# Performance work log

Measured on AMD Instinct MI355X. Metric: run time of the kernel, lower is better.

The kernel has to match this reference:

```python
import jax, jax.numpy as jnp
import numpy as np

# --- static config (matches init_kwargs) ---
N = 30000            # n_nodes
H = 8                # num_heads
OT = 16              # out_time_dim
OS = 240             # out_space_dim
IN_DIM = 16 + 1 + 240   # in_time+1 + in_space = 257
OUT_DIM = OT + 1 + OS   # 257 per head
BETA = -1.0
EPS = 1e-8
MAX_NORM = 1.0e6
SQRT_BETA = float(np.sqrt(abs(BETA)))


def setup_inputs() -> dict:
    key = jax.random.key(0)
    ks = jax.random.split(key, 7)
    def w(k, shape, fan_in):
        return (jax.random.normal(k, shape, jnp.float32) / np.sqrt(fan_in)).astype(jnp.float32)
    return {
        "query_input": jax.random.normal(ks[0], (N, IN_DIM), jnp.float32),
        "source_input": jax.random.normal(ks[1], (N, IN_DIM), jnp.float32),
        # stacked per-head PseudoLinear2 weights: [H, out, in]
        "Wq": w(ks[2], (H, OUT_DIM, IN_DIM), IN_DIM),
        "Wk": w(ks[3], (H, OUT_DIM, IN_DIM), IN_DIM),
        "Wv": w(ks[4], (H, OUT_DIM, IN_DIM), IN_DIM),
        # final head-concat projections (nn.Linear, bias=False): [out, in]
        "Ws": w(ks[5], (OT + 1, H * (OT + 1)), H * (OT + 1)),
        "Wh": w(ks[6], (OS, H * OS), H * OS),
    }


def _pseudo_linear(x, W):
    # Per-head linear; spherical block renormalized to radius sqrt(|beta|)
    # (hr output on the product manifold S^OT x H^OS). [N,D] x [H,O,D] -> [N,H,O]
    y = jnp.einsum('nd,hod->nho', x, W)
    s, sp = y[..., :OT + 1], y[..., OT + 1:]
    s = s * (SQRT_BETA / (jnp.linalg.norm(s, axis=-1, keepdims=True) + EPS))
    return jnp.concatenate([s, sp], axis=-1)


def _linear_attention(q, k, v, den_eps):
    # elu+1 feature-map linear attention; associative kv outer product per head.
    phi_q = jax.nn.elu(q) + 1.0
    phi_k = jax.nn.elu(k) + 1.0
    ktv = jnp.einsum('nhm,nhd->hmd', phi_k, v)          # [H,m,d]
    num = jnp.einsum('nhm,hmd->nhd', phi_q, ktv)        # [N,H,d]
    den = jnp.einsum('nhd,hd->nh', phi_q, phi_k.sum(0)) # [N,H]
    return num / (den[..., None] + den_eps)


def _l2norm(x):
    # torch F.normalize(p=2, dim=-1)
    return x / jnp.clip(jnp.linalg.norm(x, axis=-1, keepdims=True), 1e-12)


def reference(query_input, source_input, Wq, Wk, Wv, Ws, Wh):
    q = _pseudo_linear(query_input, Wq)   # [N,H,257]
    k = _pseudo_linear(source_input, Wk)
    v = _pseudo_linear(source_input, Wv)
    qs, qh = q[..., :OT + 1], q[..., OT + 1:]
    ks_, kh = k[..., :OT + 1], k[..., OT + 1:]
    vs, vh = v[..., :OT + 1], v[..., OT + 1:]

    # ---- spherical linear attention ----
    a = _linear_attention(qs, ks_, vs, 1e-6)            # [N,H,OT+1]
    a = a.reshape(N, H * (OT + 1)) @ Ws.T               # heads_concat
    an = jnp.linalg.norm(a, axis=-1, keepdims=True) + EPS
    mask = (an > MAX_NORM).astype(a.dtype)
    an_c = jnp.minimum(an, MAX_NORM)
    a_ = (a / an_c) * mask + a * (1.0 - mask)
    att_s = SQRT_BETA * _l2norm(a_)                     # [N,OT+1]

    # ---- hyperbolic linear attention ----
    b = _linear_attention(qh, kh, vh, 1e-8)             # [N,H,OS]
    b = b.reshape(N, H * OS) @ Wh.T
    bn = jnp.linalg.norm(b, axis=-1, keepdims=True) + EPS
    maskb = (bn > MAX_NORM).astype(b.dtype)
    bn_c = jnp.minimum(bn, MAX_NORM)
    b_ = _l2norm(b / bn_c) * MAX_NORM
    b2 = b_ * maskb + b * (1.0 - maskb)
    bt = jnp.sqrt(bn_c ** 2 - BETA)                     # hyperbolic time coord
    att_h = jnp.concatenate([bt, b2], axis=-1)          # [N,OS+1]

    out = jnp.concatenate([att_s, att_h], axis=-1)      # [N,OT+1+OS+1]
    # sh_to_q: product S x H -> pseudo-hyperboloid Q; reverse_extrinsic_map = identity here.
    s_part, h_part = out[:, :OT + 1], out[:, OT + 1:]
    q_out = jnp.concatenate([h_part[:, :1] * s_part / SQRT_BETA, h_part[:, 1:]], axis=-1)
    return q_out  # [N, 257]
```

## Files before the change

kernel.cpp:

```cpp
#include <hip/hip_runtime.h>
#include <math.h>

typedef __bf16 bf16_t;
typedef __bf16 bf16x8 __attribute__((ext_vector_type(8)));
typedef float f32x4 __attribute__((ext_vector_type(4)));

#define H    8
#define SD   17
#define HD   240
#define KIN  257
#define KQP  288
#define SCOL 256
#define DTOT 2176
#define NTOT 30000
#define CHS  6000
#define NCS  5
#define CHPS 6144
#define CHQ  7500
#define CHQP 7552
#define NCQ  4
#define KSPLIT 16

#define BK   32

__device__ __forceinline__ float phi_elu1(float x) {
    return x > 0.f ? x + 1.f : __expf(x);
}

__device__ __forceinline__ int xcd_swz(int orig, int nwg) {
    int q = nwg >> 3, r = nwg & 7;
    int xcd = orig & 7, off = orig >> 3;
    return (xcd < r ? xcd * (q + 1) : r * (q + 1) + (xcd - r) * q) + off;
}

__device__ __forceinline__ void gl_lds16(const bf16_t* g, bf16_t* l) {
    __builtin_amdgcn_global_load_lds(
        (const __attribute__((address_space(1))) void*)g,
        (__attribute__((address_space(3))) void*)l, 16, 0, 0);
}

struct GemmP {
    const bf16_t* A; long lda; long aHead;
    const bf16_t* B; long ldb; long bHead;
    float* Cf; bf16_t* Cb; long ldc; long cHead; int atomicC;
    int M, N, K, nSplit;
};

template<int TBM, int TBN>
__global__ void __launch_bounds__(256)
k_mfma_nt(GemmP p)
{
    constexpr int FI = TBM / 32;
    constexpr int FJ = TBN / 32;
    __shared__ bf16_t As[2][TBM * BK];
    __shared__ bf16_t Bs[2][TBN * BK];
    const int t  = threadIdx.x;
    const int z  = blockIdx.z;
    const int h  = z / p.nSplit;
    const int sp = z % p.nSplit;
    const int kWin = p.K / p.nSplit;
    const int k0   = sp * kWin;
    const int nwg  = gridDim.x * gridDim.y;
    const int wg   = xcd_swz(blockIdx.y * gridDim.x + blockIdx.x, nwg);
    const int m0 = (wg % gridDim.x) * TBM;
    const int n0 = (wg / gridDim.x) * TBN;
    const bf16_t* A = p.A + (long)h * p.aHead;
    const bf16_t* B = p.B + (long)h * p.bHead;

    const int lr = t >> 2;
    const int lc = t & 3;
    const int wid  = t >> 6;
    const int lane = t & 63;
    const int wm = (wid >> 1) * (TBM / 2);
    const int wn = (wid & 1) * (TBN / 2);
    const int fr = lane & 15;
    const int fq = lane >> 4;

    f32x4 acc[FI][FJ] = {};

    auto stage = [&](int buf, int kb) {
        const int gk = kb + lc * 8;
#pragma unroll
        for (int it = 0; it < TBM / 64; ++it)
            gl_lds16(A + (long)(m0 + lr + it * 64) * p.lda + gk, &As[buf][it * 2048 + t * 8]);
#pragma unroll
        for (int it = 0; it < TBN / 64; ++it)
            gl_lds16(B + (long)(n0 + lr + it * 64) * p.ldb + gk, &Bs[buf][it * 2048 + t * 8]);
    };

    stage(0, k0);
    __syncthreads();
    int cur = 0;
    for (int kb = k0; kb < k0 + kWin; kb += BK) {
        if (kb + BK < k0 + kWin) stage(cur ^ 1, kb + BK);
        bf16x8 af[FI], bfr[FJ];
#pragma unroll
        for (int i = 0; i < FI; ++i)
            af[i] = *(const bf16x8*)(&As[cur][(wm + i * 16 + fr) * BK + fq * 8]);
#pragma unroll
        for (int j = 0; j < FJ; ++j)
            bfr[j] = *(const bf16x8*)(&Bs[cur][(wn + j * 16 + fr) * BK + fq * 8]);
#pragma unroll
        for (int i = 0; i < FI; ++i)
#pragma unroll
            for (int j = 0; j < FJ; ++j)
                acc[i][j] = __builtin_amdgcn_mfma_f32_16x16x32_bf16(af[i], bfr[j], acc[i][j], 0, 0, 0);
        __syncthreads();
        cur ^= 1;
    }

    float*  Cf = p.Cf ? p.Cf + (long)h * p.cHead : (float*)0;
    bf16_t* Cb = p.Cb ? p.Cb + (long)h * p.cHead : (bf16_t*)0;
#pragma unroll
    for (int i = 0; i < FI; ++i) {
#pragma unroll
        for (int r = 0; r < 4; ++r) {
            const int m = m0 + wm + i * 16 + fq * 4 + r;
            if (m >= p.M) continue;
#pragma unroll
            for (int j = 0; j < FJ; ++j) {
                const int n = n0 + wn + j * 16 + fr;
                if (n >= p.N) continue;
                const float v = acc[i][j][r];
                const long idx = (long)m * p.ldc + n;
                if (p.atomicC)      atomicAdd(&Cf[idx], v);
                else if (Cf)        Cf[idx] = v;
                else                Cb[idx] = (bf16_t)v;
            }
        }
    }
}

__global__ void __launch_bounds__(256)
k_mfma_kv(const bf16_t* __restrict__ A, const bf16_t* __restrict__ Bsrc,
          bf16_t* __restrict__ Tk, bf16_t* __restrict__ Tv,
          float* __restrict__ ksum, int nRows)
{
    constexpr int FI = 4, FJ = 4;
    __shared__ bf16_t As[2][128 * BK];
    __shared__ bf16_t Bs[2][128 * BK];
    const int t = threadIdx.x;
    const int nwg = gridDim.x * gridDim.y;
    const int wg  = xcd_swz(blockIdx.y * gridDim.x + blockIdx.x, nwg);
    const int m0 = (wg % gridDim.x) * 128;
    const int n0 = (wg / gridDim.x) * 128;

    const int lr = t >> 2;
    const int lc = t & 3;
    const int wid  = t >> 6;
    const int lane = t & 63;
    const int wm = (wid >> 1) * 64;
    const int wn = (wid & 1) * 64;
    const int fr = lane & 15;
    const int fq = lane >> 4;

    f32x4 acc[FI][FJ] = {};

    auto stage = [&](int buf, int kb) {
        const int gk = kb + lc * 8;
        gl_lds16(A    + (long)(m0 + lr)      * KQP + gk, &As[buf][t * 8]);
        gl_lds16(A    + (long)(m0 + lr + 64) * KQP + gk, &As[buf][2048 + t * 8]);
        gl_lds16(Bsrc + (long)(n0 + lr)      * KQP + gk, &Bs[buf][t * 8]);
        gl_lds16(Bsrc + (long)(n0 + lr + 64) * KQP + gk, &Bs[buf][2048 + t * 8]);
    };

    stage(0, 0);
    __syncthreads();
    int cur = 0;
    for (int kb = 0; kb < KQP; kb += BK) {
        if (kb + BK < KQP) stage(cur ^ 1, kb + BK);
        bf16x8 af[FI], bfr[FJ];
#pragma unroll
        for (int i = 0; i < FI; ++i)
            af[i] = *(const bf16x8*)(&As[cur][(wm + i * 16 + fr) * BK + fq * 8]);
#pragma unroll
        for (int j = 0; j < FJ; ++j)
            bfr[j] = *(const bf16x8*)(&Bs[cur][(wn + j * 16 + fr) * BK + fq * 8]);
#pragma unroll
        for (int i = 0; i < FI; ++i)
#pragma unroll
            for (int j = 0; j < FJ; ++j)
                acc[i][j] = __builtin_amdgcn_mfma_f32_16x16x32_bf16(af[i], bfr[j], acc[i][j], 0, 0, 0);
        __syncthreads();
        cur ^= 1;
    }

    const bool isKh = (m0 >= SCOL) && (m0 < DTOT);
    bf16_t* outB = (m0 < DTOT) ? (Tk + (long)m0 * CHPS)
                               : (Tv + (long)(m0 - DTOT) * CHPS);
#pragma unroll
    for (int i = 0; i < FI; ++i) {
#pragma unroll
        for (int r = 0; r < 4; ++r) {
            const int ml = wm + i * 16 + fq * 4 + r;
            bf16_t* row = outB + (long)ml * CHPS;
            float kacc = 0.f;
#pragma unroll
            for (int j = 0; j < FJ; ++j) {
                const int n = n0 + wn + j * 16 + fr;
                float v = 0.f;
                if (n < nRows) {
                    v = acc[i][j][r];
                    if (isKh) { v = phi_elu1(v); kacc += v; }
                }
                row[n] = (bf16_t)v;
            }
            if (isKh) {
                kacc += __shfl_xor(kacc, 1);
                kacc += __shfl_xor(kacc, 2);
                kacc += __shfl_xor(kacc, 4);
                kacc += __shfl_xor(kacc, 8);
                if (fr == 0) atomicAdd(&ksum[m0 + ml], kacc);
            }
        }
    }
}

__global__ void k_zero_tail(bf16_t* __restrict__ Tk, bf16_t* __restrict__ Tv)
{
    const int row = blockIdx.x;
    const int t = threadIdx.x;
    bf16_t* B = (t >= 128) ? Tv : Tk;
    B[(long)row * CHPS + (CHPS - 128) + (t & 127)] = (bf16_t)0.f;
}

__global__ void __launch_bounds__(256)
k_post_kv_t(bf16_t* __restrict__ Tk, bf16_t* __restrict__ Tv,
            float* __restrict__ ksum, int rows)
{
    const int h = blockIdx.y;
    const int n = blockIdx.x * 256 + threadIdx.x;
    const int lane = threadIdx.x & 63;
    const bool act = n < rows;
    float kv[SD], vv[SD];
    float sk = 0.f, sv = 0.f;
#pragma unroll
    for (int j = 0; j < SD; ++j) {
        kv[j] = act ? (float)Tk[(long)(h * 32 + j) * CHPS + n] : 0.f;
        vv[j] = act ? (float)Tv[(long)(h * 32 + j) * CHPS + n] : 0.f;
        sk += kv[j] * kv[j];
        sv += vv[j] * vv[j];
    }
    const float ik = 1.f / (sqrtf(sk) + 1e-8f);
    const float iv = 1.f / (sqrtf(sv) + 1e-8f);
#pragma unroll
    for (int j = 0; j < SD; ++j) {
        float pk = act ? phi_elu1(kv[j] * ik) : 0.f;
        if (act) {
            Tk[(long)(h * 32 + j) * CHPS + n] = (bf16_t)pk;
            Tv[(long)(h * 32 + j) * CHPS + n] = (bf16_t)(vv[j] * iv);
        }
        float s = pk;
#pragma unroll
        for (int off = 32; off > 0; off >>= 1) s += __shfl_down(s, off);
        if (lane == 0) atomicAdd(&ksum[h * 32 + j], s);
    }
}

__global__ void k_cast_pad(const float* __restrict__ in, bf16_t* __restrict__ out, long rows)
{
    long i = (long)blockIdx.x * 256 + threadIdx.x;
    if (i >= rows * KQP) return;
    long r = i / KQP; int k = (int)(i - r * KQP);
    out[i] = (k < KIN) ? (bf16_t)in[r * KIN + k] : (bf16_t)0.f;
}

__global__ void k_prep_proj(const float* __restrict__ W, bf16_t* __restrict__ dst)
{
    long i = (long)blockIdx.x * 256 + threadIdx.x;
    if (i >= (long)DTOT * KQP) return;
    int r = (int)(i / KQP), k = (int)(i % KQP);
    float v = 0.f;
    if (r < SCOL) {
        int h = r >> 5, j = r & 31;
        if (j < SD && k < KIN) v = W[((long)h * 257 + j) * 257 + k];
    } else {
        int rr = r - SCOL;
        int h = rr / HD, j = rr % HD;
        if (k < KIN) v = W[((long)h * 257 + SD + j) * 257 + k];
    }
    dst[i] = (bf16_t)v;
}

__global__ void k_prep_ws(const float* __restrict__ ws, bf16_t* __restrict__ out)
{
    int o = blockIdx.x; int t = threadIdx.x;
    int h = t >> 5, j = t & 31;
    float v = 0.f;
    if (o < SD && j < SD) v = ws[o * (H * SD) + h * SD + j];
    out[o * 256 + t] = (bf16_t)v;
}

__global__ void k_prep_wh(const float* __restrict__ wh, bf16_t* __restrict__ out)
{
    long i = (long)blockIdx.x * 256 + threadIdx.x;
    if (i >= 256L * 2048) return;
    int o = (int)(i / 2048), c = (int)(i % 2048);
    int h = c >> 8, j = c & 255;
    float v = 0.f;
    if (o < 240 && j < HD) v = wh[(long)o * 1920 + h * HD + j];
    out[i] = (bf16_t)v;
}

__global__ void __launch_bounds__(256)
k_post_q(bf16_t* __restrict__ Yq, const float* __restrict__ ksum, int rows)
{
    const int wid  = blockIdx.x * 4 + (threadIdx.x >> 6);
    const int lane = threadIdx.x & 63;
    const int n = wid >> 3, h = wid & 7;
    if (n >= rows) return;
    bf16_t* row = Yq + (long)n * DTOT;
    float qv = (lane < SD) ? (float)row[h * 32 + lane] : 0.f;
    float sq = qv * qv;
#pragma unroll
    for (int off = 32; off > 0; off >>= 1) sq += __shfl_down(sq, off);
    sq = __shfl(sq, 0);
    const float iq = 1.f / (sqrtf(sq) + 1e-8f);
    float pvs = (lane < SD) ? phi_elu1(qv * iq) : 0.f;
    float ds = (lane < SD) ? pvs * ksum[h * 32 + lane] : 0.f;
    float pvh[4];
    float dh = 0.f;
#pragma unroll
    for (int i = 0; i < 4; ++i) {
        int o = lane + 64 * i;
        if (o < HD) {
            pvh[i] = phi_elu1((float)row[SCOL + h * HD + o]);
            dh += pvh[i] * ksum[SCOL + h * HD + o];
        } else pvh[i] = 0.f;
    }
#pragma unroll
    for (int off = 32; off > 0; off >>= 1) {
        ds += __shfl_down(ds, off);
        dh += __shfl_down(dh, off);
    }
    ds = __shfl(ds, 0); dh = __shfl(dh, 0);
    const float ss = 1.f / (ds + 1e-6f);
    const float sh = 1.f / (dh + 1e-8f);
    if (lane < 32)
        row[h * 32 + lane] = (bf16_t)((lane < SD) ? pvs * ss : 0.f);
#pragma unroll
    for (int i = 0; i < 4; ++i) {
        int o = lane + 64 * i;
        if (o < HD) row[SCOL + h * HD + o] = (bf16_t)(pvh[i] * sh);
    }
}

__global__ void k_castf(const float* __restrict__ in, bf16_t* __restrict__ out, long n)
{
    long i = (long)blockIdx.x * 256 + threadIdx.x;
    if (i < n) out[i] = (bf16_t)in[i];
}

__global__ void __launch_bounds__(256)
k_finalize(const float* __restrict__ pre, float* __restrict__ outp, int rows)
{
    int n    = blockIdx.x * 4 + (threadIdx.x >> 6);
    int lane = threadIdx.x & 63;
    if (n >= rows) return;
    const float* rp = pre + (long)n * 257;
    float* op = outp + (long)n * 257;
    float sv = (lane < SD) ? rp[lane] : 0.f;
    float ssq = sv * sv;
    float hv[4];
    float hsq = 0.f;
#pragma unroll
    for (int i = 0; i < 4; ++i) {
        int o = lane + 64 * i;
        hv[i] = (o < HD) ? rp[SD + o] : 0.f;
        hsq += hv[i] * hv[i];
    }
#pragma unroll
    for (int off = 32; off > 0; off >>= 1) {
        ssq += __shfl_down(ssq, off);
        hsq += __shfl_down(hsq, off);
    }
    ssq = __shfl(ssq, 0); hsq = __shfl(hsq, 0);
    float an_raw = sqrtf(ssq);
    float bn_raw = sqrtf(hsq);
    float an = an_raw + 1e-8f;
    float bn = bn_raw + 1e-8f;
    bool ma = an > 1e6f;
    bool mb = bn > 1e6f;
    float an_c = fminf(an, 1e6f);
    float bn_c = fminf(bn, 1e6f);
    float na = ma ? (an_raw / an_c) : an_raw;
    na = fmaxf(na, 1e-12f);
    float inv_s = (ma ? (1.f / an_c) : 1.f) / na;
    float bt = sqrtf(bn_c * bn_c + 1.0f);
    float nb = fmaxf(bn_raw / bn_c, 1e-12f);
    float scale_b = 1e6f / (bn_c * nb);
    if (lane < SD) op[lane] = bt * (sv * inv_s);
#pragma unroll
    for (int i = 0; i < 4; ++i) {
        int o = lane + 64 * i;
        if (o < HD) op[SD + o] = mb ? hv[i] * scale_b : hv[i];
    }
}

static inline long alup(long b) { return (b + 255) & ~255L; }

extern "C" void kernel_launch(void* const* d_in, const int* in_sizes, int n_in,
                              void* d_out, int out_size, void* d_ws, size_t ws_size,
                              hipStream_t stream)
{
    const float* query  = (const float*)d_in[0];
    const float* source = (const float*)d_in[1];
    const float* Wq     = (const float*)d_in[2];
    const float* Wk     = (const float*)d_in[3];
    const float* Wv     = (const float*)d_in[4];
    const float* Ws     = (const float*)d_in[5];
    const float* Wh     = (const float*)d_in[6];
    float* out = (float*)d_out;

    char* p = (char*)d_ws;
    auto alloc = [&](long b) { char* r = p; p += alup(b); return r; };
    bf16_t* Wkvb = (bf16_t*)alloc(2L * DTOT * KQP * 2);
    bf16_t* Wqb  = (bf16_t*)alloc((long)DTOT * KQP * 2);
    bf16_t* Wsb  = (bf16_t*)alloc(64L * 256 * 2);
    bf16_t* Whb  = (bf16_t*)alloc(256L * 2048 * 2);
    bf16_t* Gfull= (bf16_t*)alloc(320L * DTOT * 2);
    float*  ktvF = (float*) alloc((8L * HD * 256 + 8L * 32 * 32) * 4);
    float*  ksum = (float*) alloc((long)DTOT * 4);
    bf16_t* ktvB = (bf16_t*)alloc((8L * HD * 256 + 8L * 32 * 32) * 2);
    bf16_t* xcb  = (bf16_t*)alloc((long)CHQP * KQP * 2);
    long tkBytes = (long)DTOT * CHPS * 2;
    char* ub = alloc(2 * tkBytes + 16L * CHPS * 2);
    bf16_t* Tk  = (bf16_t*)ub;
    bf16_t* Tv  = Tk + (long)DTOT * CHPS;
    bf16_t* Yq  = Tk;
    float*  opre= (float*)(Yq + (long)CHQP * DTOT);

    float*  ktvHf = ktvF;
    float*  ktvSf = ktvF + 8L * HD * 256;
    bf16_t* ktvHb = ktvB;
    bf16_t* ktvSb = ktvB + 8L * HD * 256;

    (void)hipMemsetAsync(ktvF, 0, (char*)(ksum + DTOT) - (char*)ktvF, stream);
    (void)hipMemsetAsync(Gfull, 0, 320L * DTOT * 2, stream);

    const unsigned gw = (unsigned)(((long)DTOT * KQP + 255) / 256);
    k_prep_proj<<<gw, 256, 0, stream>>>(Wk, Wkvb);
    k_prep_proj<<<gw, 256, 0, stream>>>(Wv, Wkvb + (long)DTOT * KQP);
    k_prep_proj<<<gw, 256, 0, stream>>>(Wq, Wqb);
    k_prep_ws<<<64, 256, 0, stream>>>(Ws, Wsb);
    k_prep_wh<<<(unsigned)((256L * 2048 + 255) / 256), 256, 0, stream>>>(Wh, Whb);

    GemmP g;

    k_zero_tail<<<DTOT, 256, 0, stream>>>(Tk, Tv);
    for (int c = 0; c < NCS; ++c) {
        const float* src = source + (long)c * CHS * KIN;
        k_cast_pad<<<(unsigned)(((long)CHS * KQP + 255) / 256), 256, 0, stream>>>(src, xcb, CHS);
        k_mfma_kv<<<dim3((2 * DTOT) / 128, (CHS + 127) / 128, 1), 256, 0, stream>>>(
            Wkvb, xcb, Tk, Tv, ksum, CHS);
        k_post_kv_t<<<dim3((CHS + 255) / 256, H), 256, 0, stream>>>(Tk, Tv, ksum, CHS);
        g = { Tk + (long)SCOL * CHPS, CHPS, (long)HD * CHPS,
              Tv + (long)SCOL * CHPS, CHPS, (long)HD * CHPS,
              ktvHf, 0, 256, (long)HD * 256, 1,  HD, HD, CHPS, KSPLIT };
        k_mfma_nt<128, 128><<<dim3(2, 2, H * KSPLIT), 256, 0, stream>>>(g);
        g = { Tk, CHPS, 32L * CHPS,  Tv, CHPS, 32L * CHPS,
              ktvSf, 0, 32, 32L * 32, 1,  32, 32, CHPS, KSPLIT };
        k_mfma_nt<64, 64><<<dim3(1, 1, H * KSPLIT), 256, 0, stream>>>(g);
    }
    k_castf<<<(unsigned)((8L * (HD * 256 + 32 * 32) + 255) / 256), 256, 0, stream>>>(
        ktvF, ktvB, 8L * (HD * 256 + 32 * 32));

    g = { Wsb, 256, 32,  ktvSb, 32, 32L * 32,  0, Gfull, DTOT, 32, 0,
          SD, 32, 32, 1 };
    k_mfma_nt<64, 64><<<dim3(1, 1, H), 256, 0, stream>>>(g);
    g = { Whb, 2048, 256,  ktvHb, 256, (long)HD * 256,
          0, Gfull + 17L * DTOT + SCOL, DTOT, HD, 0,
          HD, HD, 256, 1 };
    k_mfma_nt<64, 64><<<dim3(4, 4, H), 256, 0, stream>>>(g);

    for (int c = 0; c < NCQ; ++c) {
        const float* qsrc = query + (long)c * CHQ * KIN;
        float* orow = out + (long)c * CHQ * 257;
        k_cast_pad<<<(unsigned)(((long)CHQ * KQP + 255) / 256), 256, 0, stream>>>(qsrc, xcb, CHQ);
        g = { xcb, KQP, 0,  Wqb, KQP, 0,  0, Yq, DTOT, 0, 0,
              CHQ, DTOT, KQP, 1 };
        k_mfma_nt<128, 128><<<dim3((CHQ + 127) / 128, DTOT / 128, 1), 256, 0, stream>>>(g);
        k_post_q<<<(CHQ * H) / 4, 256, 0, stream>>>(Yq, ksum, CHQ);
        g = { Yq, DTOT, 0,  Gfull, DTOT, 0,  opre, 0, 257, 0, 0,
              CHQ, 257, DTOT, 1 };
        k_mfma_nt<64, 64><<<dim3((CHQ + 63) / 64, 5, 1), 256, 0, stream>>>(g);
        k_finalize<<<(CHQ + 3) / 4, 256, 0, stream>>>(opre, orow, CHQ);
    }
}
```

Baseline: 1.148 ms.

## Triple-buffer GEMM loads with swizzled LDS, vectorize cast and q post-processing

Both MFMA GEMM kernels move from double to triple buffering. Each step now waits on an explicit vmcnt and a single barrier instead of two __syncthreads, so global-to-LDS loads run two steps ahead of compute. An XOR swizzle on the k-chunk within each LDS row aims to remove bank conflicts on the fragment reads. Separately, the cast/pad kernel and the query post kernel switch to 8-wide bf16 vector loads and stores. The cost is more LDS per block, which may lower occupancy, and hand-written waitcnt logic that must match the number of loads issued.

After: 1.156 ms. About the same (+0.7%).

```diff
diff --git a/kernel.cpp b/kernel.cpp
--- a/kernel.cpp
+++ b/kernel.cpp
@@ -39,6 +39,11 @@
         (__attribute__((address_space(3))) void*)l, 16, 0, 0);
 }
 
+template<int N> __device__ __forceinline__ void waitvm() {
+    asm volatile("s_waitcnt vmcnt(%0)" :: "n"(N) : "memory");
+    __builtin_amdgcn_sched_barrier(0);
+}
+
 struct GemmP {
     const bf16_t* A; long lda; long aHead;
     const bf16_t* B; long ldb; long bHead;
@@ -52,8 +57,9 @@
 {
     constexpr int FI = TBM / 32;
     constexpr int FJ = TBN / 32;
-    __shared__ bf16_t As[2][TBM * BK];
-    __shared__ bf16_t Bs[2][TBN * BK];
+    constexpr int LPT = TBM / 64 + TBN / 64;
+    __shared__ bf16_t As[3][TBM * BK];
+    __shared__ bf16_t Bs[3][TBN * BK];
     const int t  = threadIdx.x;
     const int z  = blockIdx.z;
     const int h  = z / p.nSplit;
@@ -79,7 +85,7 @@
     f32x4 acc[FI][FJ] = {};
 
     auto stage = [&](int buf, int kb) {
-        const int gk = kb + lc * 8;
+        const int gk = kb + ((lc ^ ((lr >> 1) & 3)) << 3);
 #pragma unroll
         for (int it = 0; it < TBM / 64; ++it)
             gl_lds16(A + (long)(m0 + lr + it * 64) * p.lda + gk, &As[buf][it * 2048 + t * 8]);
@@ -88,25 +94,37 @@
             gl_lds16(B + (long)(n0 + lr + it * 64) * p.ldb + gk, &Bs[buf][it * 2048 + t * 8]);
     };
 
+    const int nSteps = kWin / BK;
     stage(0, k0);
-    __syncthreads();
-    int cur = 0;
-    for (int kb = k0; kb < k0 + kWin; kb += BK) {
-        if (kb + BK < k0 + kWin) stage(cur ^ 1, kb + BK);
+    if (nSteps > 1) stage(1, k0 + BK);
+    int cur = 0, pf = 2;
+#pragma unroll 1
+    for (int s = 0; s < nSteps; ++s) {
+        if (s + 1 < nSteps) waitvm<LPT>();
+        else                waitvm<0>();
+        __builtin_amdgcn_s_barrier();
+        __builtin_amdgcn_sched_barrier(0);
+        if (s + 2 < nSteps) {
+            stage(pf, k0 + (s + 2) * BK);
+            pf = (pf == 2) ? 0 : pf + 1;
+        }
         bf16x8 af[FI], bfr[FJ];
 #pragma unroll
-        for (int i = 0; i < FI; ++i)
-            af[i] = *(const bf16x8*)(&As[cur][(wm + i * 16 + fr) * BK + fq * 8]);
-#pragma unroll
-        for (int j = 0; j < FJ; ++j)
-            bfr[j] = *(const bf16x8*)(&Bs[cur][(wn + j * 16 + fr) * BK + fq * 8]);
+        for (int i = 0; i < FI; ++i) {
+            const int row = wm + i * 16 + fr;
+            af[i] = *(const bf16x8*)(&As[cur][row * BK + ((fq ^ ((row >> 1) & 3)) << 3)]);
+        }
+#pragma unroll
+        for (int j = 0; j < FJ; ++j) {
+            const int row = wn + j * 16 + fr;
+            bfr[j] = *(const bf16x8*)(&Bs[cur][row * BK + ((fq ^ ((row >> 1) & 3)) << 3)]);
+        }
 #pragma unroll
         for (int i = 0; i < FI; ++i)
 #pragma unroll
             for (int j = 0; j < FJ; ++j)
                 acc[i][j] = __builtin_amdgcn_mfma_f32_16x16x32_bf16(af[i], bfr[j], acc[i][j], 0, 0, 0);
-        __syncthreads();
-        cur ^= 1;
+        cur = (cur == 2) ? 0 : cur + 1;
     }
 
     float*  Cf = p.Cf ? p.Cf + (long)h * p.cHead : (float*)0;
@@ -137,8 +155,9 @@
           float* __restrict__ ksum, int nRows)
 {
     constexpr int FI = 4, FJ = 4;
-    __shared__ bf16_t As[2][128 * BK];
-    __shared__ bf16_t Bs[2][128 * BK];
+    constexpr int LPT = 4;
+    __shared__ bf16_t As[3][128 * BK];
+    __shared__ bf16_t Bs[3][128 * BK];
     const int t = threadIdx.x;
     const int nwg = gridDim.x * gridDim.y;
     const int wg  = xcd_swz(blockIdx.y * gridDim.x + blockIdx.x, nwg);
@@ -157,32 +176,44 @@
     f32x4 acc[FI][FJ] = {};
 
     auto stage = [&](int buf, int kb) {
-        const int gk = kb + lc * 8;
+        const int gk = kb + ((lc ^ ((lr >> 1) & 3)) << 3);
         gl_lds16(A    + (long)(m0 + lr)      * KQP + gk, &As[buf][t * 8]);
         gl_lds16(A    + (long)(m0 + lr + 64) * KQP + gk, &As[buf][2048 + t * 8]);
         gl_lds16(Bsrc + (long)(n0 + lr)      * KQP + gk, &Bs[buf][t * 8]);
         gl_lds16(Bsrc + (long)(n0 + lr + 64) * KQP + gk, &Bs[buf][2048 + t * 8]);
     };
 
+    constexpr int nSteps = KQP / BK;
     stage(0, 0);
-    __syncthreads();
-    int cur = 0;
-    for (int kb = 0; kb < KQP; kb += BK) {
-        if (kb + BK < KQP) stage(cur ^ 1, kb + BK);
+    stage(1, BK);
+    int cur = 0, pf = 2;
+#pragma unroll 1
+    for (int s = 0; s < nSteps; ++s) {
+        if (s + 1 < nSteps) waitvm<LPT>();
+        else                waitvm<0>();
+        __builtin_amdgcn_s_barrier();
+        __builtin_amdgcn_sched_barrier(0);
+        if (s + 2 < nSteps) {
+            stage(pf, (s + 2) * BK);
+            pf = (pf == 2) ? 0 : pf + 1;
+        }
         bf16x8 af[FI], bfr[FJ];
 #pragma unroll
-        for (int i = 0; i < FI; ++i)
-            af[i] = *(const bf16x8*)(&As[cur][(wm + i * 16 + fr) * BK + fq * 8]);
-#pragma unroll
-        for (int j = 0; j < FJ; ++j)
-            bfr[j] = *(const bf16x8*)(&Bs[cur][(wn + j * 16 + fr) * BK + fq * 8]);
+        for (int i = 0; i < FI; ++i) {
+            const int row = wm + i * 16 + fr;
+            af[i] = *(const bf16x8*)(&As[cur][row * BK + ((fq ^ ((row >> 1) & 3)) << 3)]);
+        }
+#pragma unroll
+        for (int j = 0; j < FJ; ++j) {
+            const int row = wn + j * 16 + fr;
+            bfr[j] = *(const bf16x8*)(&Bs[cur][row * BK + ((fq ^ ((row >> 1) & 3)) << 3)]);
+        }
 #pragma unroll
         for (int i = 0; i < FI; ++i)
 #pragma unroll
             for (int j = 0; j < FJ; ++j)
                 acc[i][j] = __builtin_amdgcn_mfma_f32_16x16x32_bf16(af[i], bfr[j], acc[i][j], 0, 0, 0);
-        __syncthreads();
-        cur ^= 1;
+        cur = (cur == 2) ? 0 : cur + 1;
     }
 
     const bool isKh = (m0 >= SCOL) && (m0 < DTOT);
@@ -260,9 +291,14 @@
 __global__ void k_cast_pad(const float* __restrict__ in, bf16_t* __restrict__ out, long rows)
 {
     long i = (long)blockIdx.x * 256 + threadIdx.x;
-    if (i >= rows * KQP) return;
-    long r = i / KQP; int k = (int)(i - r * KQP);
-    out[i] = (k < KIN) ? (bf16_t)in[r * KIN + k] : (bf16_t)0.f;
+    if (i >= rows * (KQP / 8)) return;
+    long r = i / (KQP / 8); int c8 = (int)(i - r * (KQP / 8)) * 8;
+    const float* ip = in + r * KIN + c8;
+    bf16x8 o;
+#pragma unroll
+    for (int j = 0; j < 8; ++j)
+        o[j] = (c8 + j < KIN) ? (bf16_t)ip[j] : (bf16_t)0.f;
+    *(bf16x8*)(out + r * KQP + c8) = o;
 }
 
 __global__ void k_prep_proj(const float* __restrict__ W, bf16_t* __restrict__ dst)
@@ -318,15 +354,16 @@
     const float iq = 1.f / (sqrtf(sq) + 1e-8f);
     float pvs = (lane < SD) ? phi_elu1(qv * iq) : 0.f;
     float ds = (lane < SD) ? pvs * ksum[h * 32 + lane] : 0.f;
-    float pvh[4];
+    float ph[8];
     float dh = 0.f;
-#pragma unroll
-    for (int i = 0; i < 4; ++i) {
-        int o = lane + 64 * i;
-        if (o < HD) {
-            pvh[i] = phi_elu1((float)row[SCOL + h * HD + o]);
-            dh += pvh[i] * ksum[SCOL + h * HD + o];
-        } else pvh[i] = 0.f;
+    if (lane < 30) {
+        bf16x8 hv8 = *(const bf16x8*)(row + SCOL + h * HD + lane * 8);
+        const float* kp = ksum + SCOL + h * HD + lane * 8;
+#pragma unroll
+        for (int i = 0; i < 8; ++i) {
+            ph[i] = phi_elu1((float)hv8[i]);
+            dh += ph[i] * kp[i];
+        }
     }
 #pragma unroll
     for (int off = 32; off > 0; off >>= 1) {
@@ -338,10 +375,11 @@
     const float sh = 1.f / (dh + 1e-8f);
     if (lane < 32)
         row[h * 32 + lane] = (bf16_t)((lane < SD) ? pvs * ss : 0.f);
-#pragma unroll
-    for (int i = 0; i < 4; ++i) {
-        int o = lane + 64 * i;
-        if (o < HD) row[SCOL + h * HD + o] = (bf16_t)(pvh[i] * sh);
+    if (lane < 30) {
+        bf16x8 o8;
+#pragma unroll
+        for (int i = 0; i < 8; ++i) o8[i] = (bf16_t)(ph[i] * sh);
+        *(bf16x8*)(row + SCOL + h * HD + lane * 8) = o8;
     }
 }
 
@@ -450,7 +488,7 @@
     k_zero_tail<<<DTOT, 256, 0, stream>>>(Tk, Tv);
     for (int c = 0; c < NCS; ++c) {
         const float* src = source + (long)c * CHS * KIN;
-        k_cast_pad<<<(unsigned)(((long)CHS * KQP + 255) / 256), 256, 0, stream>>>(src, xcb, CHS);
+        k_cast_pad<<<(unsigned)(((long)CHS * (KQP / 8) + 255) / 256), 256, 0, stream>>>(src, xcb, CHS);
         k_mfma_kv<<<dim3((2 * DTOT) / 128, (CHS + 127) / 128, 1), 256, 0, stream>>>(
             Wkvb, xcb, Tk, Tv, ksum, CHS);
         k_post_kv_t<<<dim3((CHS + 255) / 256, H), 256, 0, stream>>>(Tk, Tv, ksum, CHS);
@@ -476,7 +514,7 @@
     for (int c = 0; c < NCQ; ++c) {
         const float* qsrc = query + (long)c * CHQ * KIN;
         float* orow = out + (long)c * CHQ * 257;
-        k_cast_pad<<<(unsigned)(((long)CHQ * KQP + 255) / 256), 256, 0, stream>>>(qsrc, xcb, CHQ);
+        k_cast_pad<<<(unsigned)(((long)CHQ * (KQP / 8) + 255) / 256), 256, 0, stream>>>(qsrc, xcb, CHQ);
         g = { xcb, KQP, 0,  Wqb, KQP, 0,  0, Yq, DTOT, 0, 0,
               CHQ, DTOT, KQP, 1 };
         k_mfma_nt<128, 128><<<dim3((CHQ + 127) / 128, DTOT / 128, 1), 256, 0, stream>>>(g);
```
